# Kernel optimization log

Hardware: AMD Instinct MI355X
Metric: run time of the kernel (lower is better)

Reference implementation:

```python
import jax, jax.numpy as jnp
import numpy as np

D_IN = 2048
D_OUT = 2048
NUM_HEADS = 16
HEAD_DIM = D_OUT // NUM_HEADS


def setup_inputs() -> dict:
    key = jax.random.key(0)
    k_x, k_qkv, k_proj, k_b = jax.random.split(key, 4)
    x = jax.random.normal(k_x, (2, 2048, D_IN), dtype=jnp.float32)
    # torch Linear(d_in, 3*d_out, bias=False): weight [3*d_out, d_in]; store transposed [d_in, 3*d_out]
    Wqkv = jax.random.normal(k_qkv, (D_IN, 3 * D_OUT), dtype=jnp.float32) / np.sqrt(D_IN)
    Wproj = jax.random.normal(k_proj, (D_OUT, D_OUT), dtype=jnp.float32) / np.sqrt(D_OUT)
    bproj = jax.random.normal(k_b, (D_OUT,), dtype=jnp.float32) * 0.01
    return {"x": x, "Wqkv": Wqkv, "Wproj": Wproj, "bproj": bproj}


def reference(x, Wqkv, Wproj, bproj):
    B, S, _ = x.shape
    qkv = x @ Wqkv  # [B, S, 3*D_OUT]
    qkv = qkv.reshape(B, S, 3, NUM_HEADS, HEAD_DIM)
    qkv = jnp.transpose(qkv, (2, 0, 3, 1, 4))  # [3, B, H, S, Dh]
    q, k, v = qkv[0], qkv[1], qkv[2]
    scale = 1.0 / np.sqrt(HEAD_DIM).astype(np.float32)
    scores = jnp.einsum('bhqd,bhkd->bhqk', q, k) * scale  # [B, H, S, S]
    causal = jnp.tril(jnp.ones((S, S), dtype=bool))
    scores = jnp.where(causal, scores, jnp.finfo(scores.dtype).min)
    attn = jax.nn.softmax(scores, axis=-1)
    out = jnp.einsum('bhqk,bhkd->bhqd', attn, v)  # [B, H, S, Dh]
    out = jnp.transpose(out, (0, 2, 1, 3)).reshape(B, S, D_OUT)
    return out @ Wproj + bproj
```

## Files before the change

### kernel.cpp

```cpp
#include <hip/hip_runtime.h>
#include <stdint.h>

typedef __attribute__((ext_vector_type(8))) short short8;
typedef __attribute__((ext_vector_type(4))) float f32x4;
typedef __attribute__((ext_vector_type(16))) float f32x16;
typedef __attribute__((ext_vector_type(4))) unsigned short u16x4;

typedef unsigned short u16;

constexpr int S_LEN = 2048;
constexpr int DH    = 128;

__device__ __forceinline__ u16 f2bf(float f) {
    union { float f; unsigned u; } v; v.f = f;
    unsigned r = v.u + 0x7FFFu + ((v.u >> 16) & 1u);
    return (u16)(r >> 16);
}
__device__ __forceinline__ unsigned cvt_pk_bf16(float lo, float hi) {
    unsigned r;
    asm("v_cvt_pk_bf16_f32 %0, %1, %2" : "=v"(r) : "v"(lo), "v"(hi));
    return r;
}
__device__ __forceinline__ void gl_lds16(const void* g, void* l) {
    __builtin_amdgcn_global_load_lds((const __attribute__((address_space(1))) void*)g,
                                     (__attribute__((address_space(3))) void*)l,
                                     16, 0, 0);
}

__global__ __launch_bounds__(256) void convx(const float* __restrict__ src,
                                             u16* __restrict__ dst) {
    size_t i = ((size_t)blockIdx.x * 256 + threadIdx.x) * 8;
    f32x4 a = *(const f32x4*)(src + i);
    f32x4 b = *(const f32x4*)(src + i + 4);
    short8 r;
    r[0] = (short)f2bf(a[0]); r[1] = (short)f2bf(a[1]);
    r[2] = (short)f2bf(a[2]); r[3] = (short)f2bf(a[3]);
    r[4] = (short)f2bf(b[0]); r[5] = (short)f2bf(b[1]);
    r[6] = (short)f2bf(b[2]); r[7] = (short)f2bf(b[3]);
    *(short8*)(dst + i) = r;
}

__global__ __launch_bounds__(256) void convT2(const float* __restrict__ s1,
                                              u16* __restrict__ d1,
                                              const float* __restrict__ s2,
                                              u16* __restrict__ d2) {
    __shared__ u16 t[64][65];
    const int bx = blockIdx.x;
    const bool first = bx < 96;
    const float* src = first ? s1 : s2;
    u16* dst = first ? d1 : d2;
    const int cols = first ? 6144 : 2048;
    const int c0 = (first ? bx : bx - 96) * 64;
    const int r0 = blockIdx.y * 64;
    const int rows = 2048;
    const int tid = threadIdx.x;
    const int colq = (tid & 15) * 4;
    const int rw   = tid >> 4;
#pragma unroll
    for (int p = 0; p < 4; ++p) {
        int row = p * 16 + rw;
        f32x4 v = *(const f32x4*)(src + (size_t)(r0 + row) * cols + c0 + colq);
        t[colq + 0][row] = f2bf(v[0]);
        t[colq + 1][row] = f2bf(v[1]);
        t[colq + 2][row] = f2bf(v[2]);
        t[colq + 3][row] = f2bf(v[3]);
    }
    __syncthreads();
    const int rowq = (tid & 15) * 4;
    const int cw   = tid >> 4;
#pragma unroll
    for (int p = 0; p < 4; ++p) {
        int col = p * 16 + cw;
        u16x4 o;
        o[0] = t[col][rowq + 0]; o[1] = t[col][rowq + 1];
        o[2] = t[col][rowq + 2]; o[3] = t[col][rowq + 3];
        *(u16x4*)(dst + (size_t)(c0 + col) * rows + r0 + rowq) = o;
    }
}

__global__ __launch_bounds__(512, 2) void gemm_qkv(
        const u16* __restrict__ A, const u16* __restrict__ BT,
        u16* __restrict__ Qo, u16* __restrict__ Ko, u16* __restrict__ VTo) {
    __shared__ __align__(16) u16 lA[3][128 * 64];
    __shared__ __align__(16) u16 lB[3][256 * 64];
    const int tid = threadIdx.x;
    const int lane = tid & 63, wave = tid >> 6;
    const int quad = lane >> 4, l16 = lane & 15;
    const int wr = wave >> 2, wc = wave & 3;
    const int m0 = blockIdx.y * 128, n0 = blockIdx.x * 256;
    const int sw = l16 & 7;
    const int c4 = tid & 7;
    f32x4 acc[4][4] = {};

    auto stageA = [&](int t1, int nb) {
#pragma unroll
        for (int j = 0; j < 2; ++j) {
            int idx = j * 512 + tid;
            int row = idx >> 3;
            gl_lds16(A + (size_t)(m0 + row) * 2048 + t1 * 64 + ((c4 ^ (row & 7)) * 8),
                     &lA[nb][row * 64 + c4 * 8]);
        }
    };
    auto stageB = [&](int h, int t1, int nb) {
#pragma unroll
        for (int j = 0; j < 2; ++j) {
            int rih = (j * 512 + tid) >> 3;
            int row = (rih & 31) + h * 32 + (rih >> 5) * 64;
            gl_lds16(BT + (size_t)(n0 + row) * 2048 + t1 * 64 + ((c4 ^ (row & 7)) * 8),
                     &lB[nb][row * 64 + c4 * 8]);
        }
    };

    stageA(0, 0); stageB(0, 0, 0); stageB(1, 0, 0);
    stageA(1, 1); stageB(0, 1, 1); stageB(1, 1, 1);

    constexpr int NT = 32;
    int buf = 0, nb2 = 2;
    for (int t = 0; t < NT; ++t) {
        const bool pf = (t + 2 < NT);
        if (t < NT - 1) asm volatile("s_waitcnt vmcnt(6)\n\ts_barrier" ::: "memory");
        else            asm volatile("s_waitcnt vmcnt(0)\n\ts_barrier" ::: "memory");
        short8 af[4][2], bfr[4][2];
        const int abase = (wr * 64 + l16) * 64;
        const int bbase = (wc * 64 + l16) * 64;
#pragma unroll
        for (int m = 0; m < 4; ++m)
#pragma unroll
            for (int ks = 0; ks < 2; ++ks)
                af[m][ks] = *(const short8*)&lA[buf][abase + m * 1024 + (((ks * 4 + quad) ^ sw)) * 8];
#pragma unroll
        for (int n = 0; n < 4; ++n)
#pragma unroll
            for (int ks = 0; ks < 2; ++ks)
                bfr[n][ks] = *(const short8*)&lB[buf][bbase + n * 1024 + (((ks * 4 + quad) ^ sw)) * 8];
        if (pf) { stageA(t + 2, nb2); stageB(0, t + 2, nb2); stageB(1, t + 2, nb2); }
        __builtin_amdgcn_s_setprio(1);
#pragma unroll
        for (int m = 0; m < 4; ++m)
#pragma unroll
            for (int n = 0; n < 4; ++n)
#pragma unroll
                for (int ks = 0; ks < 2; ++ks)
                    acc[m][n] = __builtin_amdgcn_mfma_f32_16x16x32_bf16(
                        af[m][ks], bfr[n][ks], acc[m][n], 0, 0, 0);
        __builtin_amdgcn_s_setprio(0);
        buf = (buf == 2) ? 0 : buf + 1;
        nb2 = (nb2 == 2) ? 0 : nb2 + 1;
    }

#pragma unroll
    for (int m = 0; m < 4; ++m) {
        int r0r = m0 + wr * 64 + m * 16 + quad * 4;
        int b = r0r >> 11, s0 = r0r & 2047;
#pragma unroll
        for (int n = 0; n < 4; ++n) {
            int cc = n0 + wc * 64 + n * 16 + l16;
            int which = cc >> 11, hd = (cc >> 7) & 15, dh = cc & 127;
            if (which < 2) {
                u16* dst = which == 0 ? Qo : Ko;
#pragma unroll
                for (int rg = 0; rg < 4; ++rg)
                    dst[(size_t)((b * 16 + hd) * 2048 + s0 + rg) * 128 + dh] = f2bf(acc[m][n][rg]);
            } else {
                u16x4 v;
#pragma unroll
                for (int rg = 0; rg < 4; ++rg) v[rg] = f2bf(acc[m][n][rg]);
                *(u16x4*)&VTo[((size_t)(b * 16 + hd) * 128 + dh) * 2048 + s0] = v;
            }
        }
    }
}

__global__ __launch_bounds__(256, 2) void attn_kern(
        const u16* __restrict__ Qp, const u16* __restrict__ Kp,
        const u16* __restrict__ VTp, u16* __restrict__ Ob) {
    __shared__ __align__(16) u16 lK[2][64 * 128];
    __shared__ __align__(16) u16 lV[2][128 * 64];
    const int tid = threadIdx.x, lane = tid & 63, wave = tid >> 6;
    const int ql = lane & 31, hi = lane >> 5;
    const int id = blockIdx.x;
    const int bh = id >> 4;
    const int a0 = (id + (id >> 8)) & 15;
    const int qb = (a0 & 1) ? (a0 >> 1) : (15 - (a0 >> 1));
    const int qbase = qb * 128 + wave * 32;
    const int qmax = qbase + 31;
    const int nkt = 2 * qb + 2;
    const u16* Qh = Qp + (size_t)bh * S_LEN * DH;
    const u16* Kh = Kp + (size_t)bh * S_LEN * DH;
    const u16* VTh = VTp + (size_t)bh * DH * S_LEN;

    short8 qf[8];
#pragma unroll
    for (int c = 0; c < 8; ++c)
        qf[c] = *(const short8*)&Qh[(size_t)(qbase + ql) * 128 + c * 16 + hi * 8];

    f32x16 acc[4] = {};
    float mrun = -1e30f, lrun = 0.f;
    const float SC = 0.08838834764831845f * 1.44269504088896f;

    auto stageK = [&](int kt, int b) {
        const u16* ks = Kh + (size_t)kt * 64 * 128;
#pragma unroll
        for (int p = 0; p < 4; ++p) {
            int slot = p * 256 + tid;
            int row = slot >> 4, c4 = slot & 15;
            gl_lds16(ks + row * 128 + ((c4 ^ (row & 15)) * 8), &lK[b][slot * 8]);
        }
    };
    auto stageV = [&](int kt, int b) {
        const u16* vs = VTh + kt * 64;
#pragma unroll
        for (int p = 0; p < 4; ++p) {
            int slot = p * 256 + tid;
            int row = slot >> 3, c4 = slot & 7;
            gl_lds16(vs + (size_t)row * 2048 + ((c4 ^ (row & 7)) * 8), &lV[b][slot * 8]);
        }
    };

    stageK(0, 0);
    stageV(0, 0);
    asm volatile("s_waitcnt vmcnt(4)\n\ts_barrier" ::: "memory");

    for (int kt = 0; kt < nkt; ++kt) {
        const int buf = kt & 1;
        const bool more = kt + 1 < nkt;
        const bool compute = (kt * 64 <= qmax);
        float pv0[16], pv1[16];
        if (compute) {
            const bool part = (kt * 64 + 63 > qbase);
            f32x16 s0 = {}, s1 = {};
            __builtin_amdgcn_s_setprio(1);
#pragma unroll
            for (int c = 0; c < 8; ++c) {
                int sl = ((c * 2 + hi) ^ (ql & 15)) * 8;
                short8 k0 = *(const short8*)&lK[buf][ql * 128 + sl];
                short8 k1 = *(const short8*)&lK[buf][(32 + ql) * 128 + sl];
                s0 = __builtin_amdgcn_mfma_f32_32x32x16_bf16(k0, qf[c], s0, 0, 0, 0);
                s1 = __builtin_amdgcn_mfma_f32_32x32x16_bf16(k1, qf[c], s1, 0, 0, 0);
            }
            __builtin_amdgcn_s_setprio(0);
            if (more) stageK(kt + 1, buf ^ 1);
            float pm = -1e30f;
            const int qg = qbase + ql;
            if (part) {
#pragma unroll
                for (int r = 0; r < 16; ++r) {
                    int krow = (r & 3) + 8 * (r >> 2) + 4 * hi;
                    float a = s0[r] * SC;
                    float b = s1[r] * SC;
                    if (kt * 64 + krow > qg)      a = -1e30f;
                    if (kt * 64 + 32 + krow > qg) b = -1e30f;
                    pv0[r] = a; pv1[r] = b;
                    pm = fmaxf(pm, fmaxf(a, b));
                }
            } else {
#pragma unroll
                for (int r = 0; r < 16; ++r) {
                    float a = s0[r] * SC;
                    float b = s1[r] * SC;
                    pv0[r] = a; pv1[r] = b;
                    pm = fmaxf(pm, fmaxf(a, b));
                }
            }
            pm = fmaxf(pm, __shfl_xor(pm, 32));
            if (__any(pm - mrun > 8.f)) {
                float mn = fmaxf(mrun, pm);
                float al = exp2f(mrun - mn);
                mrun = mn;
                lrun *= al;
#pragma unroll
                for (int r = 0; r < 16; ++r) {
                    float ar = __shfl(al, (r & 3) + 8 * (r >> 2) + 4 * hi);
#pragma unroll
                    for (int dc = 0; dc < 4; ++dc)
                        acc[dc][r] *= ar;
                }
            }
            float rs = 0.f;
#pragma unroll
            for (int r = 0; r < 16; ++r) {
                pv0[r] = exp2f(pv0[r] - mrun);
                pv1[r] = exp2f(pv1[r] - mrun);
                rs += pv0[r] + pv1[r];
            }
            rs += __shfl_xor(rs, 32);
            lrun += rs;
        } else if (more) {
            stageK(kt + 1, buf ^ 1);
        }
        if (more) asm volatile("s_waitcnt vmcnt(4)\n\ts_barrier" ::: "memory");
        else      asm volatile("s_waitcnt vmcnt(0)\n\ts_barrier" ::: "memory");
        if (compute) {
            unsigned X0[8], X1[8];
#pragma unroll
            for (int i = 0; i < 8; ++i) {
                X0[i] = cvt_pk_bf16(pv0[2 * i], pv0[2 * i + 1]);
                X1[i] = cvt_pk_bf16(pv1[2 * i], pv1[2 * i + 1]);
            }
            short8 pa[4];
#pragma unroll
            for (int t = 0; t < 2; ++t)
#pragma unroll
                for (int h = 0; h < 2; ++h) {
                    unsigned x0 = t ? X1[4 * h + 0] : X0[4 * h + 0];
                    unsigned x1 = t ? X1[4 * h + 1] : X0[4 * h + 1];
                    unsigned x2 = t ? X1[4 * h + 2] : X0[4 * h + 2];
                    unsigned x3 = t ? X1[4 * h + 3] : X0[4 * h + 3];
                    unsigned sx0 = (unsigned)__shfl_xor((int)x0, 32);
                    unsigned sx1 = (unsigned)__shfl_xor((int)x1, 32);
                    unsigned sx2 = (unsigned)__shfl_xor((int)x2, 32);
                    unsigned sx3 = (unsigned)__shfl_xor((int)x3, 32);
                    union { unsigned u[4]; short8 s; } uf;
                    uf.u[0] = hi ? sx2 : x0;
                    uf.u[1] = hi ? sx3 : x1;
                    uf.u[2] = hi ? x2 : sx0;
                    uf.u[3] = hi ? x3 : sx1;
                    pa[t * 2 + h] = uf.s;
                }
            __builtin_amdgcn_s_setprio(1);
#pragma unroll
            for (int dc = 0; dc < 4; ++dc) {
                const int rv = dc * 32 + ql;
#pragma unroll
                for (int kc = 0; kc < 4; ++kc) {
                    short8 vf = *(const short8*)&lV[buf][rv * 64 + (((kc * 2 + hi) ^ (ql & 7)) * 8)];
                    acc[dc] = __builtin_amdgcn_mfma_f32_32x32x16_bf16(pa[kc], vf, acc[dc], 0, 0, 0);
                }
            }
            __builtin_amdgcn_s_setprio(0);
        }
        if (more) {
            stageV(kt + 1, buf ^ 1);
            asm volatile("s_waitcnt vmcnt(4)\n\ts_barrier" ::: "memory");
        }
    }

    const int bb = bh >> 4, hh = bh & 15;
    u16* Oh = Ob + (size_t)bb * 2048 * 2048 + (size_t)hh * 128;
    float linv = 1.f / lrun;
#pragma unroll
    for (int r = 0; r < 16; ++r) {
        int qr = (r & 3) + 8 * (r >> 2) + 4 * hi;
        float lr = __shfl(linv, qr);
        int qq = qbase + qr;
#pragma unroll
        for (int dc = 0; dc < 4; ++dc)
            Oh[(size_t)qq * 2048 + dc * 32 + ql] = f2bf(acc[dc][r] * lr);
    }
}

__global__ __launch_bounds__(256, 2) void gemm_proj(
        const u16* __restrict__ Ob, const u16* __restrict__ BT,
        const float* __restrict__ bias, float* __restrict__ out) {
    __shared__ __align__(16) u16 lA[2][128 * 64];
    __shared__ __align__(16) u16 lB[2][128 * 64];
    const int tid = threadIdx.x;
    const int lane = tid & 63, wave = tid >> 6;
    const int quad = lane >> 4, l16 = lane & 15;
    const int wm = wave >> 1, wn = wave & 1;
    const int bid = blockIdx.x;
    const int swz = (bid & 7) * 64 + (bid >> 3);
    const int m0 = (swz >> 4) * 128, n0 = (swz & 15) * 128;
    const int sw = l16 & 7;
    const int c4 = tid & 7;
    f32x4 acc[4][4] = {};

    auto stageA = [&](int t1, int nb) {
#pragma unroll
        for (int j = 0; j < 4; ++j) {
            int row = (j * 256 + tid) >> 3;
            gl_lds16(Ob + (size_t)(m0 + row) * 2048 + t1 * 64 + ((c4 ^ (row & 7)) * 8),
                     &lA[nb][row * 64 + c4 * 8]);
        }
    };
    auto stageB = [&](int h, int t1, int nb) {
#pragma unroll
        for (int j = 0; j < 2; ++j) {
            int rih = (j * 256 + tid) >> 3;
            int row = (rih & 31) + h * 32 + (rih >> 5) * 64;
            gl_lds16(BT + (size_t)(n0 + row) * 2048 + t1 * 64 + ((c4 ^ (row & 7)) * 8),
                     &lB[nb][row * 64 + c4 * 8]);
        }
    };

    stageB(0, 0, 0);
    asm volatile("" ::: "memory");
    stageA(0, 0);
    asm volatile("" ::: "memory");
    stageB(1, 0, 0);

    constexpr int NT = 32;
    for (int t = 0; t < NT; ++t) {
        const int buf = t & 1, nb = buf ^ 1;
        const bool pf = (t + 1 < NT);
        asm volatile("s_waitcnt vmcnt(2)\n\ts_barrier" ::: "memory");
        short8 af[4][2], bf0[2][2];
        const int abase = (wm * 64 + l16) * 64;
        const int bbase = (wn * 64 + l16) * 64;
#pragma unroll
        for (int m = 0; m < 4; ++m)
#pragma unroll
            for (int ks = 0; ks < 2; ++ks)
                af[m][ks] = *(const short8*)&lA[buf][abase + m * 1024 + (((ks * 4 + quad) ^ sw)) * 8];
#pragma unroll
        for (int n = 0; n < 2; ++n)
#pragma unroll
            for (int ks = 0; ks < 2; ++ks)
                bf0[n][ks] = *(const short8*)&lB[buf][bbase + n * 1024 + (((ks * 4 + quad) ^ sw)) * 8];
        if (pf) {
            stageB(0, t + 1, nb);
            asm volatile("" ::: "memory");
            stageA(t + 1, nb);
        }
        __builtin_amdgcn_s_setprio(1);
#pragma unroll
        for (int m = 0; m < 4; ++m)
#pragma unroll
            for (int n = 0; n < 2; ++n)
#pragma unroll
                for (int ks = 0; ks < 2; ++ks)
                    acc[m][n] = __builtin_amdgcn_mfma_f32_16x16x32_bf16(
                        af[m][ks], bf0[n][ks], acc[m][n], 0, 0, 0);
        __builtin_amdgcn_s_setprio(0);
        if (pf) asm volatile("s_waitcnt vmcnt(6)\n\ts_barrier" ::: "memory");
        else    asm volatile("s_waitcnt vmcnt(0)\n\ts_barrier" ::: "memory");
        short8 bf1[2][2];
#pragma unroll
        for (int n = 0; n < 2; ++n)
#pragma unroll
            for (int ks = 0; ks < 2; ++ks)
                bf1[n][ks] = *(const short8*)&lB[buf][bbase + 2048 + n * 1024 + (((ks * 4 + quad) ^ sw)) * 8];
        if (pf) stageB(1, t + 1, nb);
        __builtin_amdgcn_s_setprio(1);
#pragma unroll
        for (int m = 0; m < 4; ++m)
#pragma unroll
            for (int n = 0; n < 2; ++n)
#pragma unroll
                for (int ks = 0; ks < 2; ++ks)
                    acc[m][n + 2] = __builtin_amdgcn_mfma_f32_16x16x32_bf16(
                        af[m][ks], bf1[n][ks], acc[m][n + 2], 0, 0, 0);
        __builtin_amdgcn_s_setprio(0);
    }

#pragma unroll
    for (int m = 0; m < 4; ++m) {
        int r0r = m0 + wm * 64 + m * 16 + quad * 4;
#pragma unroll
        for (int n = 0; n < 4; ++n) {
            int cc = n0 + wn * 64 + n * 16 + l16;
            float bv = bias[cc];
#pragma unroll
            for (int rg = 0; rg < 4; ++rg)
                out[(size_t)(r0r + rg) * 2048 + cc] = acc[m][n][rg] + bv;
        }
    }
}

extern "C" void kernel_launch(void* const* d_in, const int* in_sizes, int n_in,
                              void* d_out, int out_size, void* d_ws, size_t ws_size,
                              hipStream_t stream) {
    const float *x = nullptr, *Wqkv = nullptr, *Wproj = nullptr, *bproj = nullptr;
    for (int i = 0; i < n_in; ++i) {
        int sz = in_sizes[i];
        if      (sz == 2 * 2048 * 2048) x     = (const float*)d_in[i];
        else if (sz == 2048 * 6144)     Wqkv  = (const float*)d_in[i];
        else if (sz == 2048 * 2048)     Wproj = (const float*)d_in[i];
        else if (sz == 2048)            bproj = (const float*)d_in[i];
    }
    float* out = (float*)d_out;

    u16* xb     = (u16*)d_ws;
    u16* WqkvT  = xb    + (size_t)4096 * 2048;
    u16* Qb     = WqkvT + (size_t)6144 * 2048;
    u16* Kb     = Qb    + (size_t)32 * 2048 * 128;
    u16* VTb    = Kb    + (size_t)32 * 2048 * 128;
    u16* WprojT = VTb   + (size_t)32 * 2048 * 128;
    u16* Obuf   = xb;

    convx<<<dim3(4096), dim3(256), 0, stream>>>(x, xb);
    convT2<<<dim3(128, 32), dim3(256), 0, stream>>>(Wqkv, WqkvT, Wproj, WprojT);
    gemm_qkv<<<dim3(24, 32), dim3(512), 0, stream>>>(xb, WqkvT, Qb, Kb, VTb);
    attn_kern<<<dim3(512), dim3(256), 0, stream>>>(Qb, Kb, VTb, Obuf);
    gemm_proj<<<dim3(512), dim3(256), 0, stream>>>(Obuf, WprojT, bproj, out);
}
```

Measured before the change: 368.9 us.

## Enlarge proj GEMM tile to 128x256 with triple-buffered LDS; remap attention grid

The output projection GEMM goes from 256-thread 128x128 tiles with a split two-phase B load to 512-thread 128x256 tiles. It adds a three-stage LDS ring that prefetches two k-steps ahead, so each barrier covers all of a step's MMAs. The goal is more reuse per A load, fewer barriers and deeper latency hiding, at the cost of much more shared memory per block and half as many blocks. The attention grid changes from a swizzled 1D launch to 2D (bh, q-block), with heavy q-blocks scheduled first. This drops the previous head interleaving, which may change load balance and L2 locality.

```diff
diff --git a/kernel.cpp b/kernel.cpp
--- a/kernel.cpp
+++ b/kernel.cpp
@@ -178,10 +178,8 @@
     __shared__ __align__(16) u16 lV[2][128 * 64];
     const int tid = threadIdx.x, lane = tid & 63, wave = tid >> 6;
     const int ql = lane & 31, hi = lane >> 5;
-    const int id = blockIdx.x;
-    const int bh = id >> 4;
-    const int a0 = (id + (id >> 8)) & 15;
-    const int qb = (a0 & 1) ? (a0 >> 1) : (15 - (a0 >> 1));
+    const int qb = (blockIdx.y < 8) ? (15 - (int)blockIdx.y) : ((int)blockIdx.y - 8);
+    const int bh = blockIdx.x;
     const int qbase = qb * 128 + wave * 32;
     const int qmax = qbase + 31;
     const int nkt = 2 * qb + 2;
@@ -349,26 +347,25 @@
     }
 }
 
-__global__ __launch_bounds__(256, 2) void gemm_proj(
+__global__ __launch_bounds__(512, 2) void gemm_proj(
         const u16* __restrict__ Ob, const u16* __restrict__ BT,
         const float* __restrict__ bias, float* __restrict__ out) {
-    __shared__ __align__(16) u16 lA[2][128 * 64];
-    __shared__ __align__(16) u16 lB[2][128 * 64];
+    __shared__ __align__(16) u16 lA[3][128 * 64];
+    __shared__ __align__(16) u16 lB[3][256 * 64];
     const int tid = threadIdx.x;
     const int lane = tid & 63, wave = tid >> 6;
     const int quad = lane >> 4, l16 = lane & 15;
-    const int wm = wave >> 1, wn = wave & 1;
-    const int bid = blockIdx.x;
-    const int swz = (bid & 7) * 64 + (bid >> 3);
-    const int m0 = (swz >> 4) * 128, n0 = (swz & 15) * 128;
+    const int wr = wave >> 2, wc = wave & 3;
+    const int m0 = blockIdx.y * 128, n0 = blockIdx.x * 256;
     const int sw = l16 & 7;
     const int c4 = tid & 7;
     f32x4 acc[4][4] = {};
 
     auto stageA = [&](int t1, int nb) {
 #pragma unroll
-        for (int j = 0; j < 4; ++j) {
-            int row = (j * 256 + tid) >> 3;
+        for (int j = 0; j < 2; ++j) {
+            int idx = j * 512 + tid;
+            int row = idx >> 3;
             gl_lds16(Ob + (size_t)(m0 + row) * 2048 + t1 * 64 + ((c4 ^ (row & 7)) * 8),
                      &lA[nb][row * 64 + c4 * 8]);
         }
@@ -376,79 +373,56 @@
     auto stageB = [&](int h, int t1, int nb) {
 #pragma unroll
         for (int j = 0; j < 2; ++j) {
-            int rih = (j * 256 + tid) >> 3;
+            int rih = (j * 512 + tid) >> 3;
             int row = (rih & 31) + h * 32 + (rih >> 5) * 64;
             gl_lds16(BT + (size_t)(n0 + row) * 2048 + t1 * 64 + ((c4 ^ (row & 7)) * 8),
                      &lB[nb][row * 64 + c4 * 8]);
         }
     };
 
-    stageB(0, 0, 0);
-    asm volatile("" ::: "memory");
-    stageA(0, 0);
-    asm volatile("" ::: "memory");
-    stageB(1, 0, 0);
+    stageA(0, 0); stageB(0, 0, 0); stageB(1, 0, 0);
+    stageA(1, 1); stageB(0, 1, 1); stageB(1, 1, 1);
 
     constexpr int NT = 32;
+    int buf = 0, nb2 = 2;
     for (int t = 0; t < NT; ++t) {
-        const int buf = t & 1, nb = buf ^ 1;
-        const bool pf = (t + 1 < NT);
-        asm volatile("s_waitcnt vmcnt(2)\n\ts_barrier" ::: "memory");
-        short8 af[4][2], bf0[2][2];
-        const int abase = (wm * 64 + l16) * 64;
-        const int bbase = (wn * 64 + l16) * 64;
+        const bool pf = (t + 2 < NT);
+        if (t < NT - 1) asm volatile("s_waitcnt vmcnt(6)\n\ts_barrier" ::: "memory");
+        else            asm volatile("s_waitcnt vmcnt(0)\n\ts_barrier" ::: "memory");
+        short8 af[4][2], bfr[4][2];
+        const int abase = (wr * 64 + l16) * 64;
+        const int bbase = (wc * 64 + l16) * 64;
 #pragma unroll
         for (int m = 0; m < 4; ++m)
 #pragma unroll
             for (int ks = 0; ks < 2; ++ks)
                 af[m][ks] = *(const short8*)&lA[buf][abase + m * 1024 + (((ks * 4 + quad) ^ sw)) * 8];
 #pragma unroll
-        for (int n = 0; n < 2; ++n)
+        for (int n = 0; n < 4; ++n)
 #pragma unroll
             for (int ks = 0; ks < 2; ++ks)
-                bf0[n][ks] = *(const short8*)&lB[buf][bbase + n * 1024 + (((ks * 4 + quad) ^ sw)) * 8];
-        if (pf) {
-            stageB(0, t + 1, nb);
-            asm volatile("" ::: "memory");
-            stageA(t + 1, nb);
-        }
+                bfr[n][ks] = *(const short8*)&lB[buf][bbase + n * 1024 + (((ks * 4 + quad) ^ sw)) * 8];
+        if (pf) { stageA(t + 2, nb2); stageB(0, t + 2, nb2); stageB(1, t + 2, nb2); }
         __builtin_amdgcn_s_setprio(1);
 #pragma unroll
         for (int m = 0; m < 4; ++m)
 #pragma unroll
-            for (int n = 0; n < 2; ++n)
+            for (int n = 0; n < 4; ++n)
 #pragma unroll
                 for (int ks = 0; ks < 2; ++ks)
                     acc[m][n] = __builtin_amdgcn_mfma_f32_16x16x32_bf16(
-                        af[m][ks], bf0[n][ks], acc[m][n], 0, 0, 0);
+                        af[m][ks], bfr[n][ks], acc[m][n], 0, 0, 0);
         __builtin_amdgcn_s_setprio(0);
-        if (pf) asm volatile("s_waitcnt vmcnt(6)\n\ts_barrier" ::: "memory");
-        else    asm volatile("s_waitcnt vmcnt(0)\n\ts_barrier" ::: "memory");
-        short8 bf1[2][2];
-#pragma unroll
-        for (int n = 0; n < 2; ++n)
-#pragma unroll
-            for (int ks = 0; ks < 2; ++ks)
-                bf1[n][ks] = *(const short8*)&lB[buf][bbase + 2048 + n * 1024 + (((ks * 4 + quad) ^ sw)) * 8];
-        if (pf) stageB(1, t + 1, nb);
-        __builtin_amdgcn_s_setprio(1);
-#pragma unroll
-        for (int m = 0; m < 4; ++m)
-#pragma unroll
-            for (int n = 0; n < 2; ++n)
-#pragma unroll
-                for (int ks = 0; ks < 2; ++ks)
-                    acc[m][n + 2] = __builtin_amdgcn_mfma_f32_16x16x32_bf16(
-                        af[m][ks], bf1[n][ks], acc[m][n + 2], 0, 0, 0);
-        __builtin_amdgcn_s_setprio(0);
+        buf = (buf == 2) ? 0 : buf + 1;
+        nb2 = (nb2 == 2) ? 0 : nb2 + 1;
     }
 
 #pragma unroll
     for (int m = 0; m < 4; ++m) {
-        int r0r = m0 + wm * 64 + m * 16 + quad * 4;
+        int r0r = m0 + wr * 64 + m * 16 + quad * 4;
 #pragma unroll
         for (int n = 0; n < 4; ++n) {
-            int cc = n0 + wn * 64 + n * 16 + l16;
+            int cc = n0 + wc * 64 + n * 16 + l16;
             float bv = bias[cc];
 #pragma unroll
             for (int rg = 0; rg < 4; ++rg)
@@ -481,6 +455,6 @@
     convx<<<dim3(4096), dim3(256), 0, stream>>>(x, xb);
     convT2<<<dim3(128, 32), dim3(256), 0, stream>>>(Wqkv, WqkvT, Wproj, WprojT);
     gemm_qkv<<<dim3(24, 32), dim3(512), 0, stream>>>(xb, WqkvT, Qb, Kb, VTb);
-    attn_kern<<<dim3(512), dim3(256), 0, stream>>>(Qb, Kb, VTb, Obuf);
-    gemm_proj<<<dim3(512), dim3(256), 0, stream>>>(Obuf, WprojT, bproj, out);
-}
+    attn_kern<<<dim3(32, 16), dim3(256), 0, stream>>>(Qb, Kb, VTb, Obuf);
+    gemm_proj<<<dim3(8, 32), dim3(512), 0, stream>>>(Obuf, WprojT, bproj, out);
+}
```

Result: no change. 369.2 us (+0.1%).
